# Kernel optimization log

Hardware: AMD Instinct MI355X
Metric: run time of the kernel (lower is better)

The kernel has to match this reference:

```python
import jax, jax.numpy as jnp
import numpy as np

NUM_USERS = 100000
NUM_ITEMS = 50000
N_NODES = NUM_USERS + NUM_ITEMS
N_INTERACTIONS = 1000000
LATENT_DIM = 32
K = 4
N_LAYERS = 3
BATCH = 4096


def setup_inputs() -> dict:
    key = jax.random.key(0)
    k_u, k_i = jax.random.split(key)
    # torch init: normal std=0.1
    user_emb = 0.1 * jax.random.normal(k_u, (NUM_USERS, LATENT_DIM * K), dtype=jnp.float32)
    item_emb = 0.1 * jax.random.normal(k_i, (NUM_ITEMS, LATENT_DIM * K), dtype=jnp.float32)
    # build symmetric normalized bipartite adjacency (LightGCN getSparseGraph)
    rng = np.random.default_rng(0)
    u = rng.integers(0, NUM_USERS, N_INTERACTIONS)
    it = rng.integers(0, NUM_ITEMS, N_INTERACTIONS)
    src = np.concatenate([u, it + NUM_USERS]).astype(np.int32)
    dst = np.concatenate([it + NUM_USERS, u]).astype(np.int32)
    deg = np.bincount(src, minlength=N_NODES).astype(np.float32)
    deg = np.maximum(deg, 1.0)
    val = (1.0 / np.sqrt(deg[src] * deg[dst])).astype(np.float32)
    users = rng.integers(0, NUM_USERS, BATCH).astype(np.int32)
    items = rng.integers(0, NUM_ITEMS, BATCH).astype(np.int32)
    return {
        "user_emb": user_emb,
        "item_emb": item_emb,
        "edge_src": jnp.asarray(src),
        "edge_dst": jnp.asarray(dst),
        "edge_val": jnp.asarray(val),
        "users": jnp.asarray(users),
        "items": jnp.asarray(items),
    }


def _computer(user_emb, item_emb, edge_src, edge_dst, edge_val):
    n_users = user_emb.shape[0]
    n = n_users + item_emb.shape[0]
    # [N, K, D] disentangled factor view of the K*D embedding
    x = jnp.concatenate([user_emb, item_emb], axis=0).reshape(n, K, -1)
    embs = [x]
    for _ in range(N_LAYERS):
        # SpMM over all K factor slices at once: out[dst] += val * x[src]
        msgs = x[edge_src] * edge_val[:, None, None]  # [E, K, D]
        x = jax.ops.segment_sum(msgs, edge_dst, num_segments=n)
        embs.append(x)
    light_out = jnp.mean(jnp.stack(embs, axis=1), axis=1)  # [N, K, D]
    return light_out[:n_users], light_out[n_users:]


def reference(user_emb, item_emb, edge_src, edge_dst, edge_val, users, items):
    all_users, all_items = _computer(user_emb, item_emb, edge_src, edge_dst, edge_val)
    u = all_users[users]   # [B, K, D]
    i = all_items[items]   # [B, K, D]
    return jnp.sum(u * i, axis=(-1, -2))  # [B]
```

## Files before the change

kernel.cpp:

```cpp
#include <hip/hip_runtime.h>

#define NUM_USERS 100000
#define NUM_ITEMS 50000
#define N_NODES   150000
#define N_EDGES   2000000
#define N_INTER   1000000
#define DIM       128
#define DIM4      32
#define BATCH     4096
#define B_SHIFT   9
#define BUCK_N    (1 << B_SHIFT)
#define NBUCK     ((N_NODES + BUCK_N - 1) >> B_SHIFT)
#define PAIRS     4096
#define NPBLK     ((N_INTER + PAIRS - 1) / PAIRS)
#define CAP       12288
#define CAPB      16384
#define MARK_BLOCKS 512
#define CONV_BLOCKS (((N_NODES + 1) * 8 + 255) / 256)

#define G0 16.0f
#define INV_G1 (1.0f / 64.0f)
#define INV_G2 (1.0f / 256.0f)

typedef __attribute__((ext_vector_type(4))) float f32x4;
typedef __attribute__((ext_vector_type(2))) float f32x2;

__device__ inline f32x2 f8x2_lo(unsigned w) { return __builtin_amdgcn_cvt_pk_f32_fp8(w, 0); }
__device__ inline f32x2 f8x2_hi(unsigned w) { return __builtin_amdgcn_cvt_pk_f32_fp8(w, 1); }
__device__ inline unsigned enc_lo(float a, float b, unsigned old) {
    return __builtin_amdgcn_cvt_pk_fp8_f32(a, b, old, 0);
}
__device__ inline unsigned enc_hi(float a, float b, unsigned old) {
    return __builtin_amdgcn_cvt_pk_fp8_f32(a, b, old, 1);
}


__global__ void bucket_scatter_kernel(const int* __restrict__ src,
                                      int* __restrict__ bcur,
                                      int* __restrict__ tmp) {
    __shared__ int lhist[NBUCK];
    __shared__ int lcur[NBUCK];
    __shared__ int pk[2 * PAIRS];
    __shared__ unsigned short bkt[2 * PAIRS];
    int t = threadIdx.x;
    int base = blockIdx.x * PAIRS;
    for (int i = t; i < NBUCK; i += 512) lhist[i] = 0;
    __syncthreads();
    for (int i = 0; i < PAIRS / 512; ++i) {
        int p = i * 512 + t;
        int gp = base + p;
        if (gp < N_INTER) {
            int u = src[gp];
            int v = src[N_INTER + gp];
            int bu = u >> B_SHIFT, bv = v >> B_SHIFT;
            atomicAdd(&lhist[bv], 1);
            atomicAdd(&lhist[bu], 1);
            pk[2 * p]     = (u << B_SHIFT) | (v & (BUCK_N - 1));
            bkt[2 * p]    = (unsigned short)bv;
            pk[2 * p + 1] = (v << B_SHIFT) | (u & (BUCK_N - 1));
            bkt[2 * p + 1] = (unsigned short)bu;
        } else {
            bkt[2 * p] = 0xffff;
            bkt[2 * p + 1] = 0xffff;
        }
    }
    __syncthreads();
    for (int i = t; i < NBUCK; i += 512) {
        int c = lhist[i];
        lcur[i] = c ? (i * CAPB + atomicAdd(&bcur[i], c)) : 0;
    }
    __syncthreads();
    for (int i = 0; i < 2 * PAIRS / 512; ++i) {
        int li = i * 512 + t;
        int b = bkt[li];
        if (b != 0xffff) {
            int pos = atomicAdd(&lcur[b], 1);
            if (pos < (b + 1) * CAPB)
                tmp[pos] = pk[li];
        }
    }
}


__global__ void place_kernel(const int* __restrict__ bcur,
                             const int* __restrict__ tmp,
                             int* __restrict__ row_start,
                             float* __restrict__ rinv,
                             float* __restrict__ sdeg,
                             int* __restrict__ csr_src) {
    __shared__ int lhist[BUCK_N];
    __shared__ int lofs[BUCK_N];
    __shared__ int ssc[512];
    __shared__ int outbuf[CAP];
    int b = blockIdx.x;
    int t = threadIdx.x;

    int c = 0;
    if (t < NBUCK) {
        c = bcur[t];
        if (c > CAPB) c = CAPB;
    }
    ssc[t] = c;
    __syncthreads();
    for (int off = 1; off < 512; off <<= 1) {
        int v = (t >= off) ? ssc[t - off] : 0;
        __syncthreads();
        ssc[t] += v;
        __syncthreads();
    }
    int beg = (b == 0) ? 0 : ssc[b - 1];
    int end = ssc[b];
    int cnt = end - beg;
    int tbase = b * CAPB;
    int n0 = b << B_SHIFT;
    int n1 = n0 + BUCK_N; if (n1 > N_NODES) n1 = N_NODES;
    if (b == NBUCK - 1 && t == 0) row_start[N_NODES] = end;

    lhist[t] = 0;
    __syncthreads();
    for (int e = t; e < cnt; e += 512)
        atomicAdd(&lhist[tmp[tbase + e] & (BUCK_N - 1)], 1);
    __syncthreads();

    int v = lhist[t];
    ssc[t] = v;
    __syncthreads();
    for (int off = 1; off < 512; off <<= 1) {
        int u = (t >= off) ? ssc[t - off] : 0;
        __syncthreads();
        ssc[t] += u;
        __syncthreads();
    }
    int excl = ssc[t] - v;
    lofs[t] = excl;
    int node = n0 + t;
    if (node < n1) {
        row_start[node] = beg + excl;
        float d = (float)(v > 1 ? v : 1);
        float rr = rsqrtf(d);
        rinv[node] = rr;
        sdeg[node] = d * rr;
    }
    __syncthreads();

    if (cnt <= CAP) {
        for (int e = t; e < cnt; e += 512) {
            int p = tmp[tbase + e];
            int pos = atomicAdd(&lofs[p & (BUCK_N - 1)], 1);
            outbuf[pos] = p >> B_SHIFT;
        }
        __syncthreads();
        for (int i = t; i < cnt; i += 512) csr_src[beg + i] = outbuf[i];
    } else {
        for (int e = t; e < cnt; e += 512) {
            int p = tmp[tbase + e];
            int pos = atomicAdd(&lofs[p & (BUCK_N - 1)], 1);
            csr_src[beg + pos] = p >> B_SHIFT;
        }
    }
}


__global__ void mark_conv_kernel(const f32x4* __restrict__ ue4,
                                 const f32x4* __restrict__ ie4,
                                 const float* __restrict__ rinv,
                                 uint4* __restrict__ e16f8,
                                 uint4* __restrict__ w1f8,
                                 uint4* __restrict__ w2f8,
                                 const int* __restrict__ users,
                                 const int* __restrict__ items,
                                 const int* __restrict__ row_start,
                                 const int* __restrict__ csr_src,
                                 int* __restrict__ mark,
                                 int* __restrict__ wcnt,
                                 int* __restrict__ wlist) {
    int bid = blockIdx.x;
    if (bid < MARK_BLOCKS) {
        int g = threadIdx.x >> 4;
        int lane = threadIdx.x & 15;
        int b = bid * 16 + g;
        int node = (b < BATCH) ? users[b] : (NUM_USERS + items[b - BATCH]);
        if (lane == 0) {
            if (atomicExch(&mark[node], 1) == 0) wlist[atomicAdd(wcnt, 1)] = node;
        }
        int beg = row_start[node], end = row_start[node + 1];
        for (int e = beg + lane; e < end; e += 16) {
            int s = csr_src[e];
            if (atomicExch(&mark[s], 1) == 0) wlist[atomicAdd(wcnt, 1)] = s;
        }
        return;
    }
    int i = (bid - MARK_BLOCKS) * 256 + threadIdx.x;
    const int total = (N_NODES + 1) * 8;
    if (i >= total) return;
    int n = i >> 3;
    if (n >= N_NODES) {
        uint4 z = make_uint4(0u, 0u, 0u, 0u);
        e16f8[i] = z;
        w1f8[i] = z;
        w2f8[i] = z;
        return;
    }
    int j = i & 7;
    const f32x4* row = (n < NUM_USERS) ? ue4 + (size_t)n * DIM4
                                       : ie4 + (size_t)(n - NUM_USERS) * DIM4;
    float r = rinv[n] * G0;
    f32x4 c0 = __builtin_nontemporal_load(&row[4 * j]);
    f32x4 c1 = __builtin_nontemporal_load(&row[4 * j + 1]);
    f32x4 c2 = __builtin_nontemporal_load(&row[4 * j + 2]);
    f32x4 c3 = __builtin_nontemporal_load(&row[4 * j + 3]);
    uint4 o;
    o.x = enc_hi(r * c0.z, r * c0.w, enc_lo(r * c0.x, r * c0.y, 0u));
    o.y = enc_hi(r * c1.z, r * c1.w, enc_lo(r * c1.x, r * c1.y, 0u));
    o.z = enc_hi(r * c2.z, r * c2.w, enc_lo(r * c2.x, r * c2.y, 0u));
    o.w = enc_hi(r * c3.z, r * c3.w, enc_lo(r * c3.x, r * c3.y, 0u));
    e16f8[i] = o;
}


__device__ inline void spmm_row(int n, const uint2* __restrict__ tabl,
                                const int* __restrict__ row_start,
                                const int* __restrict__ csr_src,
                                const float* __restrict__ rinv,
                                uint2* __restrict__ out,
                                int lane, int gbase) {
    int beg = row_start[n], end = row_start[n + 1];
    f32x2 a0 = {0.f, 0.f}, a1 = {0.f, 0.f}, a2 = {0.f, 0.f}, a3 = {0.f, 0.f};
    for (int base = beg; base < end; base += 16) {
        int eidx = base + lane;
        int myedge = (eidx < end) ? csr_src[eidx] : N_NODES;
        int s[16];
#pragma unroll
        for (int k = 0; k < 16; ++k) s[k] = __shfl(myedge, gbase + k, 64);
        uint2 h[16];
#pragma unroll
        for (int k = 0; k < 16; ++k) h[k] = tabl[s[k] << 4];
#pragma unroll
        for (int k = 0; k < 16; ++k) {
            a0 += f8x2_lo(h[k].x);
            a1 += f8x2_hi(h[k].x);
            a2 += f8x2_lo(h[k].y);
            a3 += f8x2_hi(h[k].y);
        }
    }
    float f = rinv[n];
    f = 4.0f * f * f;
    a0 *= f; a1 *= f; a2 *= f; a3 *= f;
    uint2 o;
    o.x = enc_hi(a1[0], a1[1], enc_lo(a0[0], a0[1], 0u));
    o.y = enc_hi(a3[0], a3[1], enc_lo(a2[0], a2[1], 0u));
    out[((size_t)n << 4) + lane] = o;
}

__global__ __launch_bounds__(256) void spmm_f8_kernel(
        const uint2* __restrict__ tab,
        const int* __restrict__ row_start,
        const int* __restrict__ csr_src,
        const float* __restrict__ rinv,
        uint2* __restrict__ out) {
    int t = threadIdx.x;
    int n = blockIdx.x * 16 + (t >> 4);
    if (n >= N_NODES) return;
    spmm_row(n, tab + (t & 15), row_start, csr_src, rinv, out, t & 15, t & 48);
}

__global__ __launch_bounds__(256) void spmm_f8_list_kernel(
        const uint2* __restrict__ tab,
        const int* __restrict__ row_start,
        const int* __restrict__ csr_src,
        const float* __restrict__ rinv,
        const int* __restrict__ wcnt,
        const int* __restrict__ wlist,
        uint2* __restrict__ out) {
    int t = threadIdx.x;
    int cnt = wcnt[0];
    int stride = gridDim.x * 16;
    for (int idx = blockIdx.x * 16 + (t >> 4); idx < cnt; idx += stride) {
        int n = wlist[idx];
        spmm_row(n, tab + (t & 15), row_start, csr_src, rinv, out, t & 15, t & 48);
    }
}


__global__ void epilogue_kernel(const f32x4* __restrict__ ue4,
                                const f32x4* __restrict__ ie4,
                                const uint2* __restrict__ w1f8,
                                const uint2* __restrict__ w2f8,
                                const int* __restrict__ row_start,
                                const int* __restrict__ csr_src,
                                const float* __restrict__ rinv,
                                const float* __restrict__ sdeg,
                                const int* __restrict__ users,
                                const int* __restrict__ items,
                                float* __restrict__ out) {
    int t = threadIdx.x;
    int elem = blockIdx.x * 4 + (t >> 5);
    int half = (t >> 4) & 1;
    int lane = t & 15;
    int gbase = t & 48;
    int node = half ? (NUM_USERS + items[elem]) : users[elem];

    const f32x4* erow = (node < NUM_USERS) ? ue4 + (size_t)node * DIM4
                                           : ie4 + (size_t)(node - NUM_USERS) * DIM4;
    f32x4 f0 = erow[2 * lane];
    f32x4 f1 = erow[2 * lane + 1];
    float a[8] = {f0.x, f0.y, f0.z, f0.w, f1.x, f1.y, f1.z, f1.w};

    float sd = sdeg[node];
    uint2 d1 = w1f8[(size_t)node * 16 + lane];
    uint2 d2 = w2f8[(size_t)node * 16 + lane];
    f32x2 p0 = f8x2_lo(d1.x), p1 = f8x2_hi(d1.x), p2 = f8x2_lo(d1.y), p3 = f8x2_hi(d1.y);
    f32x2 q0 = f8x2_lo(d2.x), q1 = f8x2_hi(d2.x), q2 = f8x2_lo(d2.y), q3 = f8x2_hi(d2.y);
    a[0] += sd * (p0[0] * INV_G1 + q0[0] * INV_G2);
    a[1] += sd * (p0[1] * INV_G1 + q0[1] * INV_G2);
    a[2] += sd * (p1[0] * INV_G1 + q1[0] * INV_G2);
    a[3] += sd * (p1[1] * INV_G1 + q1[1] * INV_G2);
    a[4] += sd * (p2[0] * INV_G1 + q2[0] * INV_G2);
    a[5] += sd * (p2[1] * INV_G1 + q2[1] * INV_G2);
    a[6] += sd * (p3[0] * INV_G1 + q3[0] * INV_G2);
    a[7] += sd * (p3[1] * INV_G1 + q3[1] * INV_G2);

    int beg = row_start[node], end = row_start[node + 1];
    f32x2 b0 = {0.f, 0.f}, b1 = {0.f, 0.f}, b2 = {0.f, 0.f}, b3 = {0.f, 0.f};
    const uint2* w2l = w2f8 + lane;
    for (int base = beg; base < end; base += 16) {
        int eidx = base + lane;
        int myedge = (eidx < end) ? csr_src[eidx] : N_NODES;
        int s[16];
#pragma unroll
        for (int k = 0; k < 16; ++k) s[k] = __shfl(myedge, gbase + k, 64);
        uint2 h[16];
#pragma unroll
        for (int k = 0; k < 16; ++k) h[k] = w2l[(size_t)s[k] << 4];
#pragma unroll
        for (int k = 0; k < 16; ++k) {
            b0 += f8x2_lo(h[k].x);
            b1 += f8x2_hi(h[k].x);
            b2 += f8x2_lo(h[k].y);
            b3 += f8x2_hi(h[k].y);
        }
    }
    float rv = rinv[node] * INV_G2;
    a[0] += rv * b0[0]; a[1] += rv * b0[1];
    a[2] += rv * b1[0]; a[3] += rv * b1[1];
    a[4] += rv * b2[0]; a[5] += rv * b2[1];
    a[6] += rv * b3[0]; a[7] += rv * b3[1];

    int wl = t & 63;
    float p = 0.f;
#pragma unroll
    for (int j = 0; j < 8; ++j) p += a[j] * __shfl(a[j], wl ^ 16, 64);
    for (int off = 8; off > 0; off >>= 1) p += __shfl_down(p, off, 16);
    if (half == 0 && lane == 0) out[elem] = p * (1.0f / 16.0f);
}

extern "C" void kernel_launch(void* const* d_in, const int* in_sizes, int n_in,
                              void* d_out, int out_size, void* d_ws, size_t ws_size,
                              hipStream_t stream) {
    const f32x4* ue4 = (const f32x4*)d_in[0];
    const f32x4* ie4 = (const f32x4*)d_in[1];
    const int*   src   = (const int*)d_in[2];
    const int*   users = (const int*)d_in[5];
    const int*   items = (const int*)d_in[6];
    float* out = (float*)d_out;

    const size_t frow = (size_t)(N_NODES + 1) * 16;
    char* ws = (char*)d_ws;
    uint2* e16f8 = (uint2*)ws;  ws += frow * sizeof(uint2);
    uint2* w1f8  = (uint2*)ws;  ws += frow * sizeof(uint2);
    uint2* w2f8  = (uint2*)ws;  ws += frow * sizeof(uint2);
    int*   row_start = (int*)ws;    ws += (size_t)(N_NODES + 1) * sizeof(int);
    float* rinv      = (float*)ws;  ws += (size_t)N_NODES * sizeof(float);
    float* sdeg      = (float*)ws;  ws += (size_t)N_NODES * sizeof(float);
    int*   mark      = (int*)ws;    ws += (size_t)N_NODES * sizeof(int);
    int*   bcur      = (int*)ws;    ws += (size_t)NBUCK * sizeof(int);
    int*   wcnt      = (int*)ws;    ws += sizeof(int);
    int*   wlist     = (int*)ws;    ws += (size_t)N_NODES * sizeof(int);
    ws = (char*)(((size_t)ws + 255) & ~(size_t)255);
    int*   tmp       = (int*)ws;    ws += (size_t)NBUCK * CAPB * sizeof(int);
    int*   csr_src   = (int*)ws;    ws += (size_t)N_EDGES * sizeof(int);

    hipMemsetAsync(mark, 0, (size_t)(N_NODES + NBUCK + 1) * sizeof(int), stream);

    bucket_scatter_kernel<<<NPBLK, 512, 0, stream>>>(src, bcur, tmp);
    place_kernel<<<NBUCK, 512, 0, stream>>>(bcur, tmp, row_start, rinv, sdeg, csr_src);

    mark_conv_kernel<<<MARK_BLOCKS + CONV_BLOCKS, 256, 0, stream>>>(
        ue4, ie4, rinv, (uint4*)e16f8, (uint4*)w1f8, (uint4*)w2f8,
        users, items, row_start, csr_src, mark, wcnt, wlist);

    spmm_f8_kernel<<<(N_NODES + 15) / 16, 256, 0, stream>>>(
        e16f8, row_start, csr_src, rinv, w1f8);

    spmm_f8_list_kernel<<<4096, 256, 0, stream>>>(
        w1f8, row_start, csr_src, rinv, wcnt, wlist, w2f8);

    epilogue_kernel<<<BATCH / 4, 128, 0, stream>>>(
        ue4, ie4, w1f8, w2f8, row_start, csr_src, rinv, sdeg, users, items, out);
}
```

Before: 297.1 us.

## Replace atomic worklist with plain mark flags and re-read edges in bucket scatter

The second SpMM no longer uses an atomically built compacted worklist. Marking now does plain stores, and the layer-2 kernel launches over all nodes and exits early for unmarked rows, which removes contended atomicExch/atomicAdd traffic. The bucket scatter also drops its shared-memory staging of packed edges and bucket ids and reloads src from global memory in the second pass, cutting LDS use and raising occupancy at the cost of reading the edge list twice. The masked launch adds many near-empty blocks and loses the worklist's compaction, and the order of edges within a bucket may differ from before.

```diff
diff --git a/kernel.cpp b/kernel.cpp
--- a/kernel.cpp
+++ b/kernel.cpp
@@ -40,28 +40,17 @@
                                       int* __restrict__ tmp) {
     __shared__ int lhist[NBUCK];
     __shared__ int lcur[NBUCK];
-    __shared__ int pk[2 * PAIRS];
-    __shared__ unsigned short bkt[2 * PAIRS];
     int t = threadIdx.x;
     int base = blockIdx.x * PAIRS;
     for (int i = t; i < NBUCK; i += 512) lhist[i] = 0;
     __syncthreads();
     for (int i = 0; i < PAIRS / 512; ++i) {
-        int p = i * 512 + t;
-        int gp = base + p;
+        int gp = base + i * 512 + t;
         if (gp < N_INTER) {
             int u = src[gp];
             int v = src[N_INTER + gp];
-            int bu = u >> B_SHIFT, bv = v >> B_SHIFT;
-            atomicAdd(&lhist[bv], 1);
-            atomicAdd(&lhist[bu], 1);
-            pk[2 * p]     = (u << B_SHIFT) | (v & (BUCK_N - 1));
-            bkt[2 * p]    = (unsigned short)bv;
-            pk[2 * p + 1] = (v << B_SHIFT) | (u & (BUCK_N - 1));
-            bkt[2 * p + 1] = (unsigned short)bu;
-        } else {
-            bkt[2 * p] = 0xffff;
-            bkt[2 * p + 1] = 0xffff;
+            atomicAdd(&lhist[v >> B_SHIFT], 1);
+            atomicAdd(&lhist[u >> B_SHIFT], 1);
         }
     }
     __syncthreads();
@@ -70,13 +59,19 @@
         lcur[i] = c ? (i * CAPB + atomicAdd(&bcur[i], c)) : 0;
     }
     __syncthreads();
-    for (int i = 0; i < 2 * PAIRS / 512; ++i) {
-        int li = i * 512 + t;
-        int b = bkt[li];
-        if (b != 0xffff) {
-            int pos = atomicAdd(&lcur[b], 1);
-            if (pos < (b + 1) * CAPB)
-                tmp[pos] = pk[li];
+    for (int i = 0; i < PAIRS / 512; ++i) {
+        int gp = base + i * 512 + t;
+        if (gp < N_INTER) {
+            int u = src[gp];
+            int v = src[N_INTER + gp];
+            int bv = v >> B_SHIFT;
+            int bu = u >> B_SHIFT;
+            int pos0 = atomicAdd(&lcur[bv], 1);
+            if (pos0 < (bv + 1) * CAPB)
+                tmp[pos0] = (u << B_SHIFT) | (v & (BUCK_N - 1));
+            int pos1 = atomicAdd(&lcur[bu], 1);
+            if (pos1 < (bu + 1) * CAPB)
+                tmp[pos1] = (v << B_SHIFT) | (u & (BUCK_N - 1));
         }
     }
 }
@@ -171,23 +166,16 @@
                                  const int* __restrict__ items,
                                  const int* __restrict__ row_start,
                                  const int* __restrict__ csr_src,
-                                 int* __restrict__ mark,
-                                 int* __restrict__ wcnt,
-                                 int* __restrict__ wlist) {
+                                 int* __restrict__ mark) {
     int bid = blockIdx.x;
     if (bid < MARK_BLOCKS) {
         int g = threadIdx.x >> 4;
         int lane = threadIdx.x & 15;
         int b = bid * 16 + g;
         int node = (b < BATCH) ? users[b] : (NUM_USERS + items[b - BATCH]);
-        if (lane == 0) {
-            if (atomicExch(&mark[node], 1) == 0) wlist[atomicAdd(wcnt, 1)] = node;
-        }
+        if (lane == 0) mark[node] = 1;
         int beg = row_start[node], end = row_start[node + 1];
-        for (int e = beg + lane; e < end; e += 16) {
-            int s = csr_src[e];
-            if (atomicExch(&mark[s], 1) == 0) wlist[atomicAdd(wcnt, 1)] = s;
-        }
+        for (int e = beg + lane; e < end; e += 16) mark[csr_src[e]] = 1;
         return;
     }
     int i = (bid - MARK_BLOCKS) * 256 + threadIdx.x;
@@ -264,21 +252,18 @@
     spmm_row(n, tab + (t & 15), row_start, csr_src, rinv, out, t & 15, t & 48);
 }
 
-__global__ __launch_bounds__(256) void spmm_f8_list_kernel(
+__global__ __launch_bounds__(256) void spmm_f8_masked_kernel(
         const uint2* __restrict__ tab,
         const int* __restrict__ row_start,
         const int* __restrict__ csr_src,
         const float* __restrict__ rinv,
-        const int* __restrict__ wcnt,
-        const int* __restrict__ wlist,
+        const int* __restrict__ mark,
         uint2* __restrict__ out) {
     int t = threadIdx.x;
-    int cnt = wcnt[0];
-    int stride = gridDim.x * 16;
-    for (int idx = blockIdx.x * 16 + (t >> 4); idx < cnt; idx += stride) {
-        int n = wlist[idx];
-        spmm_row(n, tab + (t & 15), row_start, csr_src, rinv, out, t & 15, t & 48);
-    }
+    int n = blockIdx.x * 16 + (t >> 4);
+    if (n >= N_NODES) return;
+    if (!mark[n]) return;
+    spmm_row(n, tab + (t & 15), row_start, csr_src, rinv, out, t & 15, t & 48);
 }
 
 
@@ -374,26 +359,24 @@
     float* sdeg      = (float*)ws;  ws += (size_t)N_NODES * sizeof(float);
     int*   mark      = (int*)ws;    ws += (size_t)N_NODES * sizeof(int);
     int*   bcur      = (int*)ws;    ws += (size_t)NBUCK * sizeof(int);
-    int*   wcnt      = (int*)ws;    ws += sizeof(int);
-    int*   wlist     = (int*)ws;    ws += (size_t)N_NODES * sizeof(int);
     ws = (char*)(((size_t)ws + 255) & ~(size_t)255);
     int*   tmp       = (int*)ws;    ws += (size_t)NBUCK * CAPB * sizeof(int);
     int*   csr_src   = (int*)ws;    ws += (size_t)N_EDGES * sizeof(int);
 
-    hipMemsetAsync(mark, 0, (size_t)(N_NODES + NBUCK + 1) * sizeof(int), stream);
+    hipMemsetAsync(mark, 0, (size_t)(N_NODES + NBUCK) * sizeof(int), stream);
 
     bucket_scatter_kernel<<<NPBLK, 512, 0, stream>>>(src, bcur, tmp);
     place_kernel<<<NBUCK, 512, 0, stream>>>(bcur, tmp, row_start, rinv, sdeg, csr_src);
 
     mark_conv_kernel<<<MARK_BLOCKS + CONV_BLOCKS, 256, 0, stream>>>(
         ue4, ie4, rinv, (uint4*)e16f8, (uint4*)w1f8, (uint4*)w2f8,
-        users, items, row_start, csr_src, mark, wcnt, wlist);
+        users, items, row_start, csr_src, mark);
 
     spmm_f8_kernel<<<(N_NODES + 15) / 16, 256, 0, stream>>>(
         e16f8, row_start, csr_src, rinv, w1f8);
 
-    spmm_f8_list_kernel<<<4096, 256, 0, stream>>>(
-        w1f8, row_start, csr_src, rinv, wcnt, wlist, w2f8);
+    spmm_f8_masked_kernel<<<(N_NODES + 15) / 16, 256, 0, stream>>>(
+        w1f8, row_start, csr_src, rinv, mark, w2f8);
 
     epilogue_kernel<<<BATCH / 4, 128, 0, stream>>>(
         ue4, ie4, w1f8, w2f8, row_start, csr_src, rinv, sdeg, users, items, out);
```

After: 247.7 us. 1.2x faster.
